# Optimization experiments

Measured on AMD Instinct MI355X. Metric: run time of the kernel, lower is better.

## Reference

```python
import jax, jax.numpy as jnp
import numpy as np

# fp4 e2m1 positive value grid and midpoints between adjacent grid values
_GRID = jnp.array([0.0, 0.5, 1.0, 1.5, 2.0, 3.0, 4.0, 6.0], dtype=jnp.float32)
_MIDS = jnp.array([0.25, 0.75, 1.25, 1.75, 2.5, 3.5, 5.0], dtype=jnp.float32)
BLOCK = 32               # MX block size
E8M0_BIAS = 127
F32_MIN_NORMAL = float(2.0 ** -126)
F4_E2M1_MAX_POW2 = 2     # log2 of largest power-of-two <= 6.0 -> 4.0


def _quantize_fp4(a):
    """Round-to-nearest-even onto the signed e2m1 grid."""
    mag = jnp.clip(jnp.abs(a), 0.0, 6.0)
    idx = jnp.searchsorted(_MIDS, mag, side='left')  # ties round down
    mids_pad = jnp.concatenate([_MIDS, jnp.array([-1.0], jnp.float32)])
    tie = mag == mids_pad[idx]
    idx = jnp.where(tie & (idx % 2 == 1), idx + 1, idx)  # ties-to-even mantissa
    return _GRID[idx] * jnp.where(a < 0, -1.0, 1.0)


def _floor_log2(m):
    """Exact floor(log2(m)) for m > 0, with corrections for fp rounding of log2."""
    e = jnp.floor(jnp.log2(m))
    e = jnp.where(jnp.exp2(e) > m, e - 1.0, e)
    e = jnp.where(jnp.exp2(e + 1.0) <= m, e + 1.0, e)
    return e


def _qdq_mxfp4(x):
    """Quantize-dequantize x to MX fp4_e2m1, block 32, FLOOR scale mode (to_mx + to_dtype)."""
    shp = x.shape
    xb = x.reshape(-1, BLOCK)
    max_abs = jnp.max(jnp.abs(xb), axis=1)
    eps = F32_MIN_NORMAL * (max_abs == 0).astype(jnp.float32)
    pow2 = _floor_log2(max_abs + eps)
    e_unb = jnp.clip(pow2 - F4_E2M1_MAX_POW2, -float(E8M0_BIAS), float(E8M0_BIAS) + 1.0)
    scale = jnp.maximum(jnp.exp2(e_unb), F32_MIN_NORMAL)  # [nblk]
    q = _quantize_fp4(xb / scale[:, None])
    return (q * scale[:, None]).reshape(shp)


def _dequant_weight(weight_packed, weight_scale, out_f, in_f):
    """Unpack uint8-packed fp4 (low nibble first), apply e8m0 block scales."""
    p = weight_packed.astype(jnp.int32)
    low = p & 0xF
    high = (p >> 4) & 0xF
    nib = jnp.stack([low, high], axis=-1).reshape(out_f, in_f)  # interleave low,high
    vals = _GRID[nib & 7] * jnp.where((nib & 8) > 0, -1.0, 1.0)
    s = jnp.exp2(weight_scale.astype(jnp.float32) - E8M0_BIAS)  # get_fp_scale(e8m0)
    return (vals.reshape(-1, BLOCK) * s[:, None]).reshape(out_f, in_f)


def setup_inputs() -> dict:
    key = jax.random.key(0)
    k1, k2, k3 = jax.random.split(key, 3)
    M, IN, OUT = 4096, 4096, 4096
    x = jax.random.normal(k1, (M, IN), dtype=jnp.float32)
    weight_packed = jax.random.randint(k2, (OUT, IN // 2), 0, 256, dtype=jnp.int32)
    weight_scale = jax.random.randint(k3, (OUT * IN // BLOCK,), 0, 135, dtype=jnp.int32)
    return {"x": x, "weight_packed": weight_packed, "weight_scale": weight_scale}


def reference(x, weight_packed, weight_scale):
    out_f = weight_packed.shape[0]
    in_f = weight_packed.shape[1] * 2
    xq = _qdq_mxfp4(x)                                       # qdq_mxfp4(x)
    w_dq = _dequant_weight(weight_packed, weight_scale, out_f, in_f)
    return xq @ w_dq.T                                       # matmul(x, w_dq.t())
```

## Files before the change

kernel.cpp:

```cpp
#include <hip/hip_runtime.h>
#include <stdint.h>

typedef __attribute__((ext_vector_type(4)))  int   intx4;
typedef __attribute__((ext_vector_type(8)))  int   intx8;
typedef __attribute__((ext_vector_type(16))) float floatx16;

#define GLL16(gp, lp)                                                               \
    __builtin_amdgcn_global_load_lds((const __attribute__((address_space(1))) unsigned int*)(gp), \
                                     (__attribute__((address_space(3))) unsigned int*)(lp), 16, 0, 0)
#define GLL4(gp, lp)                                                                \
    __builtin_amdgcn_global_load_lds((const __attribute__((address_space(1))) unsigned int*)(gp), \
                                     (__attribute__((address_space(3))) unsigned int*)(lp), 4, 0, 0)

__device__ __forceinline__ uint32_t enc1(float xv, float inv) {
    float a = fminf(fabsf(xv) * inv, 6.0f);
    int e;
    if (a < 2.0f)      e = (int)rintf(a + a);
    else if (a < 4.0f) e = (int)rintf(a) + 2;
    else               e = (int)rintf(a * 0.5f) + 4;
    return (uint32_t)e | ((__float_as_uint(xv) >> 28) & 8u);
}

__global__ __launch_bounds__(256) void quant_x_kernel(const float* __restrict__ x,
                                                      uint32_t* __restrict__ xq,
                                                      uint8_t* __restrict__ xs) {
    const int gl = blockIdx.x * 256 + threadIdx.x;
    const float4 v = ((const float4*)x)[gl];
    float m = fmaxf(fmaxf(fabsf(v.x), fabsf(v.y)), fmaxf(fabsf(v.z), fabsf(v.w)));
    m = fmaxf(m, __shfl_xor(m, 1));
    m = fmaxf(m, __shfl_xor(m, 2));
    m = fmaxf(m, __shfl_xor(m, 4));
    const unsigned ef = __float_as_uint(m) >> 23;
    const unsigned code = (ef < 3u) ? 1u : (ef - 2u);
    const float inv = __uint_as_float((254u - code) << 23);
    const uint32_t p = enc1(v.x, inv)        | (enc1(v.y, inv) << 4)
                     | (enc1(v.z, inv) << 8) | (enc1(v.w, inv) << 12);
    ((uint16_t*)xq)[gl] = (uint16_t)p;
    if ((gl & 7) == 0) xs[gl >> 3] = (uint8_t)code;
}

__global__ __launch_bounds__(256) void repack_kernel(const int* __restrict__ wp,
                                                     uint32_t* __restrict__ wrep,
                                                     int n4w,
                                                     const int* __restrict__ wsc,
                                                     uint32_t* __restrict__ ws,
                                                     int n4s) {
    const int t = blockIdx.x * 256 + threadIdx.x;
    if (t < n4w) {
        const int4 p = ((const int4*)wp)[t];
        wrep[t] = (uint32_t)(p.x & 0xFF) | ((uint32_t)(p.y & 0xFF) << 8)
                | ((uint32_t)(p.z & 0xFF) << 16) | ((uint32_t)(p.w & 0xFF) << 24);
    } else if (t - n4w < n4s) {
        const int i = t - n4w;
        const int4 p = ((const int4*)wsc)[i];
        ws[i] = (uint32_t)(p.x & 0xFF) | ((uint32_t)(p.y & 0xFF) << 8)
              | ((uint32_t)(p.z & 0xFF) << 16) | ((uint32_t)(p.w & 0xFF) << 24);
    }
}

__global__ __launch_bounds__(256) void gemm_mx_kernel(const uint8_t* __restrict__ Apk,
                                                      const uint8_t* __restrict__ Bpk,
                                                      const uint8_t* __restrict__ As,
                                                      const uint8_t* __restrict__ Bs,
                                                      float* __restrict__ C,
                                                      int M, int N, int K) {
    __shared__ __align__(16) uint8_t sA[8192];
    __shared__ __align__(16) uint8_t sB[8192];
    __shared__ __align__(16) uint8_t sS[1024];

    const int tid = threadIdx.x;
    const int bm0 = blockIdx.y << 7;
    const int bn0 = blockIdx.x << 7;
    const int wave = tid >> 6;
    const int lane = tid & 63;
    const int wm = (wave >> 1) << 6;
    const int wn = (wave & 1) << 6;
    const int row = lane & 31;
    const int h = lane >> 5;
    const int Kb = K >> 1;
    const int kbpr = K >> 5;

    const int s0 = tid, s1 = tid + 256;
    const int r0 = s0 >> 2, p0 = (s0 & 3) ^ ((r0 >> 1) & 3);
    const int r1 = s1 >> 2, p1 = (s1 & 3) ^ ((r1 >> 1) & 3);
    const uint8_t* Ag0 = Apk + (size_t)(bm0 + r0) * Kb + p0 * 16;
    const uint8_t* Ag1 = Apk + (size_t)(bm0 + r1) * Kb + p1 * 16;
    const uint8_t* Bg0 = Bpk + (size_t)(bn0 + r0) * Kb + p0 * 16;
    const uint8_t* Bg1 = Bpk + (size_t)(bn0 + r1) * Kb + p1 * 16;

    const int srow = tid & 127;
    const uint8_t* Sg = (tid < 128) ? (As + (size_t)(bm0 + srow) * kbpr)
                                    : (Bs + (size_t)(bn0 + srow) * kbpr);
    const int sldoff = ((tid < 128) ? 0 : 512) + srow * 4;

    floatx16 acc[2][2];
#pragma unroll
    for (int a = 0; a < 2; ++a)
#pragma unroll
        for (int b = 0; b < 2; ++b)
#pragma unroll
            for (int r = 0; r < 16; ++r) acc[a][b][r] = 0.f;

    const int nchunk = K >> 7;
    const int ar0 = wm + row, ar1 = wm + 32 + row;
    const int br0 = wn + row, br1 = wn + 32 + row;

    for (int c = 0; c < nchunk; ++c) {
        __syncthreads();
        const size_t koff = (size_t)c << 6;
        GLL16(Ag0 + koff, sA + s0 * 16);
        GLL16(Ag1 + koff, sA + s1 * 16);
        GLL16(Bg0 + koff, sB + s0 * 16);
        GLL16(Bg1 + koff, sB + s1 * 16);
        GLL4(Sg + (size_t)c * 4, sS + sldoff);
        __syncthreads();

#pragma unroll
        for (int s = 0; s < 2; ++s) {
            const int kp = 2 * s + h;
            intx4 a4[2], b4[2];
            int sa[2], sb[2];
            a4[0] = *(const intx4*)(sA + ar0 * 64 + ((kp ^ ((ar0 >> 1) & 3)) << 4));
            a4[1] = *(const intx4*)(sA + ar1 * 64 + ((kp ^ ((ar1 >> 1) & 3)) << 4));
            b4[0] = *(const intx4*)(sB + br0 * 64 + ((kp ^ ((br0 >> 1) & 3)) << 4));
            b4[1] = *(const intx4*)(sB + br1 * 64 + ((kp ^ ((br1 >> 1) & 3)) << 4));
            sa[0] = sS[ar0 * 4 + kp];
            sa[1] = sS[ar1 * 4 + kp];
            sb[0] = sS[512 + br0 * 4 + kp];
            sb[1] = sS[512 + br1 * 4 + kp];
#pragma unroll
            for (int mt = 0; mt < 2; ++mt)
#pragma unroll
                for (int nt = 0; nt < 2; ++nt) {
                    intx8 a8 = {a4[mt][0], a4[mt][1], a4[mt][2], a4[mt][3], 0, 0, 0, 0};
                    intx8 b8 = {b4[nt][0], b4[nt][1], b4[nt][2], b4[nt][3], 0, 0, 0, 0};
                    acc[mt][nt] = __builtin_amdgcn_mfma_scale_f32_32x32x64_f8f6f4(
                        a8, b8, acc[mt][nt], 4, 4, 0, sa[mt], 0, sb[nt]);
                }
        }
    }

#pragma unroll
    for (int mt = 0; mt < 2; ++mt)
#pragma unroll
        for (int nt = 0; nt < 2; ++nt) {
            const int col = bn0 + wn + nt * 32 + row;
#pragma unroll
            for (int g = 0; g < 4; ++g) {
                const int rw = bm0 + wm + mt * 32 + 8 * g + 4 * h;
#pragma unroll
                for (int q = 0; q < 4; ++q)
                    C[(size_t)(rw + q) * N + col] = acc[mt][nt][4 * g + q];
            }
        }
}

extern "C" void kernel_launch(void* const* d_in, const int* in_sizes, int n_in,
                              void* d_out, int out_size, void* d_ws, size_t ws_size,
                              hipStream_t stream) {
    const float* x = (const float*)d_in[0];
    const int* wp = (const int*)d_in[1];
    const int* wsc = (const int*)d_in[2];
    float* out = (float*)d_out;

    const int K = 4096;
    const int M = in_sizes[0] / K;
    const int N = (in_sizes[1] * 2) / K;
    const int kbpr = K / 32;
    const int npack = N * K / 2;

    uint32_t* xq   = (uint32_t*)d_ws;
    uint8_t*  xs   = (uint8_t*)d_ws + (size_t)M * K / 2;
    uint8_t*  ws   = xs + (size_t)M * kbpr;
    uint32_t* wrep = (uint32_t*)(ws + (size_t)N * kbpr);

    const int n4w = npack / 4;
    const int n4s = (N * kbpr) / 4;

    quant_x_kernel<<<(M * K / 4) / 256, 256, 0, stream>>>(x, xq, xs);
    repack_kernel<<<(n4w + n4s + 255) / 256, 256, 0, stream>>>(wp, wrep, n4w,
                                                               wsc, (uint32_t*)ws, n4s);

    dim3 grid(N / 128, M / 128);
    gemm_mx_kernel<<<grid, 256, 0, stream>>>((const uint8_t*)xq, (const uint8_t*)wrep,
                                             xs, ws, out, M, N, K);
}
```

Before: 212.6 us.

## Transpose block scales to K-major layout for coalesced scale loads in GEMM

Adds a kernel that transposes the per-block e8m0 scales of both the quantized activations and the weights, so that scales for consecutive rows at the same K block sit contiguously. The GEMM's per-chunk scale load then reads 4 contiguous bytes per thread across rows instead of 4 bytes strided by the row pitch. The shared-memory scale lookup is re-indexed to match. This costs an extra kernel launch and a pass over the scales, and relies on xs and ws being adjacent in the workspace, since the transpose treats them as one 2M-row array and assumes M equals N.

```diff
diff --git a/kernel.cpp b/kernel.cpp
--- a/kernel.cpp
+++ b/kernel.cpp
@@ -58,10 +58,39 @@
     }
 }
 
+__global__ __launch_bounds__(256) void tpose_s_kernel(const uint8_t* __restrict__ nat,
+                                                      uint8_t* __restrict__ xs_t,
+                                                      uint8_t* __restrict__ ws_t,
+                                                      int R, int Ck) {
+    __shared__ uint8_t raw[128 * 32];
+    const int r0 = blockIdx.x * 128;
+    const int c0 = blockIdx.y * 32;
+    const int t = threadIdx.x;
+    {
+        const int r = t >> 1, hf = t & 1;
+        const uint4 v = *(const uint4*)(nat + (size_t)(r0 + r) * Ck + c0 + hf * 16);
+        *(uint4*)(raw + r * 32 + hf * 16) = v;
+    }
+    __syncthreads();
+    const int c = t >> 3, q = t & 7;
+    uint32_t d[4];
+#pragma unroll
+    for (int j = 0; j < 4; ++j) {
+        const int mb = q * 16 + j * 4;
+        d[j] = (uint32_t)raw[(mb + 0) * 32 + c]
+             | ((uint32_t)raw[(mb + 1) * 32 + c] << 8)
+             | ((uint32_t)raw[(mb + 2) * 32 + c] << 16)
+             | ((uint32_t)raw[(mb + 3) * 32 + c] << 24);
+    }
+    uint8_t* outp = (r0 < R) ? (xs_t + (size_t)(c0 + c) * R + r0)
+                             : (ws_t + (size_t)(c0 + c) * R + (r0 - R));
+    *(uint4*)(outp + q * 16) = make_uint4(d[0], d[1], d[2], d[3]);
+}
+
 __global__ __launch_bounds__(256) void gemm_mx_kernel(const uint8_t* __restrict__ Apk,
                                                       const uint8_t* __restrict__ Bpk,
-                                                      const uint8_t* __restrict__ As,
-                                                      const uint8_t* __restrict__ Bs,
+                                                      const uint8_t* __restrict__ AsT,
+                                                      const uint8_t* __restrict__ BsT,
                                                       float* __restrict__ C,
                                                       int M, int N, int K) {
     __shared__ __align__(16) uint8_t sA[8192];
@@ -78,7 +107,6 @@
     const int row = lane & 31;
     const int h = lane >> 5;
     const int Kb = K >> 1;
-    const int kbpr = K >> 5;
 
     const int s0 = tid, s1 = tid + 256;
     const int r0 = s0 >> 2, p0 = (s0 & 3) ^ ((r0 >> 1) & 3);
@@ -88,10 +116,12 @@
     const uint8_t* Bg0 = Bpk + (size_t)(bn0 + r0) * Kb + p0 * 16;
     const uint8_t* Bg1 = Bpk + (size_t)(bn0 + r1) * Kb + p1 * 16;
 
-    const int srow = tid & 127;
-    const uint8_t* Sg = (tid < 128) ? (As + (size_t)(bm0 + srow) * kbpr)
-                                    : (Bs + (size_t)(bn0 + srow) * kbpr);
-    const int sldoff = ((tid < 128) ? 0 : 512) + srow * 4;
+    const int st = tid & 127;
+    const int sj = st >> 5, si = st & 31;
+    const uint8_t* Sg = (tid < 128) ? (AsT + (size_t)sj * M + bm0 + si * 4)
+                                    : (BsT + (size_t)sj * N + bn0 + si * 4);
+    uint8_t* Sl = sS + ((tid < 128) ? 0 : 512) + st * 4;
+    const size_t sAdv = (size_t)4 * (size_t)((tid < 128) ? M : N);
 
     floatx16 acc[2][2];
 #pragma unroll
@@ -112,7 +142,7 @@
         GLL16(Ag1 + koff, sA + s1 * 16);
         GLL16(Bg0 + koff, sB + s0 * 16);
         GLL16(Bg1 + koff, sB + s1 * 16);
-        GLL4(Sg + (size_t)c * 4, sS + sldoff);
+        GLL4(Sg + (size_t)c * sAdv, Sl);
         __syncthreads();
 
 #pragma unroll
@@ -124,10 +154,10 @@
             a4[1] = *(const intx4*)(sA + ar1 * 64 + ((kp ^ ((ar1 >> 1) & 3)) << 4));
             b4[0] = *(const intx4*)(sB + br0 * 64 + ((kp ^ ((br0 >> 1) & 3)) << 4));
             b4[1] = *(const intx4*)(sB + br1 * 64 + ((kp ^ ((br1 >> 1) & 3)) << 4));
-            sa[0] = sS[ar0 * 4 + kp];
-            sa[1] = sS[ar1 * 4 + kp];
-            sb[0] = sS[512 + br0 * 4 + kp];
-            sb[1] = sS[512 + br1 * 4 + kp];
+            sa[0] = sS[kp * 128 + ar0];
+            sa[1] = sS[kp * 128 + ar1];
+            sb[0] = sS[512 + kp * 128 + br0];
+            sb[1] = sS[512 + kp * 128 + br1];
 #pragma unroll
             for (int mt = 0; mt < 2; ++mt)
 #pragma unroll
@@ -173,6 +203,8 @@
     uint8_t*  xs   = (uint8_t*)d_ws + (size_t)M * K / 2;
     uint8_t*  ws   = xs + (size_t)M * kbpr;
     uint32_t* wrep = (uint32_t*)(ws + (size_t)N * kbpr);
+    uint8_t*  xs_t = (uint8_t*)(wrep + (size_t)npack / 4);
+    uint8_t*  ws_t = xs_t + (size_t)M * kbpr;
 
     const int n4w = npack / 4;
     const int n4s = (N * kbpr) / 4;
@@ -180,8 +212,10 @@
     quant_x_kernel<<<(M * K / 4) / 256, 256, 0, stream>>>(x, xq, xs);
     repack_kernel<<<(n4w + n4s + 255) / 256, 256, 0, stream>>>(wp, wrep, n4w,
                                                                wsc, (uint32_t*)ws, n4s);
+    dim3 tg(2 * M / 128, kbpr / 32);
+    tpose_s_kernel<<<tg, 256, 0, stream>>>(xs, xs_t, ws_t, M, kbpr);
 
     dim3 grid(N / 128, M / 128);
     gemm_mx_kernel<<<grid, 256, 0, stream>>>((const uint8_t*)xq, (const uint8_t*)wrep,
-                                             xs, ws, out, M, N, K);
-}
+                                             xs_t, ws_t, out, M, N, K);
+}
```

Result: faster. 193.0 us (-9.2%).
